# Kernel optimization log

Measured on AMD Instinct MI355X. Metric: run time of the kernel, lower is better.

## Reference

```python
import jax, jax.numpy as jnp
import numpy as np

B, A, D, H, F = 256, 96, 384, 192, 96   # molecules, atoms, feat, hidden, species-MLP out
S = 4                                   # number of species (H, C, N, O)
E = B * A * 32                          # edges (avg degree 32)
CUTOFF = 5.2


def smooth_cutoff(d, cutoff):
    # Smoothstep-style cutoff: 1 at d=0, smoothly -> 0 at d=cutoff (Smoothstep class, reversed edges)
    x = jnp.clip((cutoff - d) / cutoff, 0.0, 1.0)
    return x ** 3 * (x * (6.0 * x - 15.0) + 10.0)


def setup_inputs() -> dict:
    key = jax.random.key(0)
    ks = jax.random.split(key, 9)
    species = jax.random.randint(ks[0], (B, A), 0, S, dtype=jnp.int32)
    in_features = jax.random.normal(ks[1], (B, A, D), dtype=jnp.float32)
    atom_index12 = jax.random.randint(ks[2], (2, E), 0, B * A, dtype=jnp.int32)
    distances = jax.random.uniform(ks[3], (E,), jnp.float32, 0.1, CUTOFF)
    total_charges = jnp.zeros((B,), jnp.float32)
    W1 = jax.random.normal(ks[4], (S, D, H), jnp.float32) / np.float32(np.sqrt(D))
    W2 = jax.random.normal(ks[5], (S, H, F), jnp.float32) / np.float32(np.sqrt(H))
    Wn = jax.random.normal(ks[6], (S, F, F), jnp.float32) / np.float32(np.sqrt(F))
    Wf = jax.random.normal(ks[7], (S, 2 * F, 1), jnp.float32) / np.float32(np.sqrt(2 * F))
    return dict(species=species, in_features=in_features, atom_index12=atom_index12,
                distances=distances, total_charges=total_charges,
                W1=W1, W2=W2, Wn=Wn, Wf=Wf,
                decay_prefactor=jnp.asarray(1.0, jnp.float32),
                decay_factor=jnp.asarray(1.0, jnp.float32))


def reference(species, in_features, atom_index12, distances, total_charges,
              W1, W2, Wn, Wf, decay_prefactor, decay_factor):
    b, a, d = in_features.shape
    n = b * a
    sp = species.reshape(-1)                      # [N]
    x = in_features.reshape(n, d)                 # [N, D]

    # per-species main MLP dispatch: internal[i] = MLP_{sp[i]}(x[i])
    internal = jnp.zeros((n, F), x.dtype)
    for s in range(S):
        mask = (sp == s)[:, None]
        h = jax.nn.gelu(x @ W1[s]) @ W2[s]        # [N, F]
        internal = internal + jnp.where(mask, h, jnp.zeros((), x.dtype))

    # per-species neighbor MLP
    nbr = jnp.zeros((n, F), x.dtype)
    for s in range(S):
        mask = (sp == s)[:, None]
        nbr = nbr + jnp.where(mask, internal @ Wn[s], jnp.zeros((), x.dtype))

    # distance-decayed edge messages: merged[i0] += nbr[i1]*w, merged[i1] += nbr[i0]*w
    decay = (decay_prefactor ** 2) * jnp.exp(-(decay_factor ** 2) * distances) \
            * smooth_cutoff(distances, CUTOFF)    # [E]
    i0, i1 = atom_index12[0], atom_index12[1]
    m_to_i0 = nbr[i1] * decay[:, None]            # [E, F]
    m_to_i1 = nbr[i0] * decay[:, None]
    merged = jax.ops.segment_sum(jnp.concatenate([m_to_i0, m_to_i1], axis=0),
                                 jnp.concatenate([i0, i1], axis=0),
                                 num_segments=n)  # [N, F]

    feats = jnp.concatenate([internal, merged], axis=-1)  # [N, 2F]

    # per-species final head -> precharges
    precharges = jnp.zeros((n,), x.dtype)
    for s in range(S):
        mask = (sp == s)
        precharges = precharges + jnp.where(mask, (feats @ Wf[s])[:, 0], jnp.zeros((), x.dtype))
    precharges = precharges.reshape(b, a)

    # total-charge redistribution (uniform factors, no learned redistribution)
    dummy_mask = species != -1
    factors = 1.0 / dummy_mask.sum(-1, keepdims=True).astype(x.dtype)
    charges = precharges + (total_charges - precharges.sum(-1))[:, None] * factors
    charges = jnp.where(dummy_mask, charges, jnp.zeros((), x.dtype))
    return species, charges, precharges
```

## Files before the change

kernel.cpp:

```cpp
#include <hip/hip_runtime.h>
#include <cstdint>
#include <cstddef>

#define NBm 256
#define NAm 96
#define NDm 384
#define NHm 192
#define NFm 96
#define NSm 4
#define NATOMS (NBm*NAm)
#define NEe (NATOMS*32)
#define NMSG (2*NEe)
#define HBLK 1536
#define CUTOFF_ 5.2f

typedef __attribute__((ext_vector_type(8))) short short8;
typedef __attribute__((ext_vector_type(4))) float float4v;
typedef __attribute__((ext_vector_type(2))) int int2v;

__device__ __forceinline__ short f2bf(float f){
  union { float f; unsigned u; } v; v.f = f;
  unsigned r = v.u + 0x7FFFu + ((v.u >> 16) & 1u);
  return (short)(r >> 16);
}

__device__ __forceinline__ float gelu_t(float x){
  float u = 0.7978845608028654f * (x + 0.044715f * x*x*x);
  float e = __expf(-2.0f * fabsf(u));
  float t = (1.0f - e) / (1.0f + e);
  t = (u >= 0.f) ? t : -t;
  return 0.5f * x * (1.0f + t);
}

#define W1N (NSm*NDm*NHm)
#define W2N (NSm*NHm*NFm)
#define WNN (NSm*NFm*NFm)
__global__ void k_wprep(const float* __restrict__ W1, const float* __restrict__ W2,
                        const float* __restrict__ Wn,
                        short* __restrict__ W1t, short* __restrict__ W2t,
                        short* __restrict__ Wnt, int* __restrict__ spc){
  if (blockIdx.x == 0 && threadIdx.x < NSm) spc[threadIdx.x] = 0;
  int idx = blockIdx.x*256 + threadIdx.x;
  if (idx < W1N){
    int s = idx / (NDm*NHm); int rem = idx - s*NDm*NHm;
    int k = rem / NHm, c = rem - k*NHm;
    W1t[(s*NHm + c)*NDm + k] = f2bf(W1[idx]);
  } else if (idx < W1N + W2N){
    int j = idx - W1N;
    int s = j / (NHm*NFm); int rem = j - s*NHm*NFm;
    int k = rem / NFm, c = rem - k*NFm;
    W2t[(s*NFm + c)*NHm + k] = f2bf(W2[j]);
  } else if (idx < W1N + W2N + WNN){
    int j = idx - W1N - W2N;
    int s = j / (NFm*NFm); int rem = j - s*NFm*NFm;
    int k = rem / NFm, c = rem - k*NFm;
    Wnt[(s*NFm + c)*NFm + k] = f2bf(Wn[j]);
  }
}

__global__ void k_spcount(const int* __restrict__ sp, int* __restrict__ spc){
  __shared__ int h[NSm];
  int t = threadIdx.x;
  if (t < NSm) h[t] = 0;
  __syncthreads();
  int i = blockIdx.x*256 + t;
  atomicAdd(&h[sp[i]], 1);
  __syncthreads();
  if (t < NSm) atomicAdd(&spc[t], h[t]);
}

__global__ void k_spscan(const int* __restrict__ spc, int* __restrict__ sps, int* __restrict__ spcur){
  if (threadIdx.x==0 && blockIdx.x==0){
    int r=0;
    for (int s=0;s<NSm;s++){ sps[s]=r; spcur[s]=r; r+=spc[s]; }
    sps[NSm]=r;
  }
}

__global__ void k_spscatter(const int* __restrict__ sp, int* __restrict__ spcur,
                            int* __restrict__ order){
  __shared__ int h[NSm], base[NSm];
  int t = threadIdx.x;
  if (t < NSm) h[t]=0;
  __syncthreads();
  int i = blockIdx.x*256 + t;
  int s = sp[i];
  int lr = atomicAdd(&h[s], 1);
  __syncthreads();
  if (t < NSm) base[t] = atomicAdd(&spcur[t], h[t]);
  __syncthreads();
  order[base[s] + lr] = i;
}

__global__ __launch_bounds__(256) void k_mlp(
    const float* __restrict__ X, const int* __restrict__ order,
    const int* __restrict__ sps,
    const short* __restrict__ W1t, const short* __restrict__ W2t,
    const short* __restrict__ Wnt, const float* __restrict__ Wf,
    float* __restrict__ pre, float* __restrict__ nbr_g){
  const int s = blockIdx.y;
  const int s0 = sps[s];
  const int cnt = sps[s+1] - s0;
  const int row0 = blockIdx.x * 64;
  if (row0 >= cnt) return;

  __shared__ short Hs[64][200];
  __shared__ short Ws[192*40];
  __shared__ short Is[64][104];
  __shared__ int aids[64];

  const int tid = threadIdx.x;
  if (tid < 64){
    int r = row0 + tid;
    aids[tid] = order[s0 + ((r < cnt) ? r : 0)];
  }
  __syncthreads();

  const int wave = tid >> 6, lane = tid & 63;
  const int lrow = lane & 15, quad = lane >> 4;
  const int arow = wave*16 + lrow;
  const float* xrow = X + (size_t)aids[arow]*NDm + quad*8;

  short8 afs[12];
  #pragma unroll
  for (int kb=0; kb<12; kb++){
    const float* p = xrow + kb*32;
    #pragma unroll
    for (int j=0;j<8;j++) afs[kb][j] = f2bf(p[j]);
  }

  const short* W1s = W1t + (size_t)s*NHm*NDm;
  float4v acc[12];
  #pragma unroll
  for (int i=0;i<12;i++){ acc[i][0]=0.f; acc[i][1]=0.f; acc[i][2]=0.f; acc[i][3]=0.f; }

  for (int kb=0; kb<12; kb++){
    __syncthreads();
    for (int e = tid; e < 192*4; e += 256){
      int c = e >> 2, kq = (e & 3) * 8;
      *(short8*)(&Ws[c*40 + kq]) = *(const short8*)(W1s + c*NDm + kb*32 + kq);
    }
    __syncthreads();
    short8 af = afs[kb];
    #pragma unroll
    for (int ct=0; ct<12; ct++){
      short8 bfb = *(const short8*)(&Ws[(ct*16 + lrow)*40 + quad*8]);
      acc[ct] = __builtin_amdgcn_mfma_f32_16x16x32_bf16(af, bfb, acc[ct], 0,0,0);
    }
  }
  #pragma unroll
  for (int ct=0; ct<12; ct++){
    #pragma unroll
    for (int r=0;r<4;r++){
      Hs[wave*16 + quad*4 + r][ct*16 + lrow] = f2bf(gelu_t(acc[ct][r]));
    }
  }

  const short* W2s = W2t + (size_t)s*NFm*NHm;
  float4v acc2[6];
  #pragma unroll
  for (int i=0;i<6;i++){ acc2[i][0]=0.f; acc2[i][1]=0.f; acc2[i][2]=0.f; acc2[i][3]=0.f; }
  for (int kb=0; kb<6; kb++){
    __syncthreads();
    for (int e = tid; e < 96*4; e += 256){
      int c = e >> 2, kq = (e & 3) * 8;
      *(short8*)(&Ws[c*40 + kq]) = *(const short8*)(W2s + c*NHm + kb*32 + kq);
    }
    __syncthreads();
    short8 af2 = *(const short8*)(&Hs[wave*16 + lrow][kb*32 + quad*8]);
    #pragma unroll
    for (int ct=0; ct<6; ct++){
      short8 bfb = *(const short8*)(&Ws[(ct*16 + lrow)*40 + quad*8]);
      acc2[ct] = __builtin_amdgcn_mfma_f32_16x16x32_bf16(af2, bfb, acc2[ct], 0,0,0);
    }
  }
  #pragma unroll
  for (int ct=0; ct<6; ct++){
    #pragma unroll
    for (int r=0;r<4;r++){
      Is[wave*16 + quad*4 + r][ct*16 + lrow] = f2bf(acc2[ct][r]);
    }
  }

  {
    float pr[4] = {0.f,0.f,0.f,0.f};
    #pragma unroll
    for (int ct=0; ct<6; ct++){
      float wv = Wf[s*2*NFm + ct*16 + lrow];
      #pragma unroll
      for (int r=0;r<4;r++) pr[r] += acc2[ct][r] * wv;
    }
    #pragma unroll
    for (int m=1; m<16; m<<=1){
      #pragma unroll
      for (int r=0;r<4;r++) pr[r] += __shfl_xor(pr[r], m, 64);
    }
    if (lrow == 0){
      #pragma unroll
      for (int r=0;r<4;r++){
        int row = wave*16 + quad*4 + r;
        if (row0 + row < cnt) pre[aids[row]] = pr[r];
      }
    }
  }

  const short* Wns = Wnt + (size_t)s*NFm*NFm;
  float4v acc3[6];
  #pragma unroll
  for (int i=0;i<6;i++){ acc3[i][0]=0.f; acc3[i][1]=0.f; acc3[i][2]=0.f; acc3[i][3]=0.f; }
  for (int kb=0; kb<3; kb++){
    __syncthreads();
    for (int e = tid; e < 96*4; e += 256){
      int c = e >> 2, kq = (e & 3) * 8;
      *(short8*)(&Ws[c*40 + kq]) = *(const short8*)(Wns + c*NFm + kb*32 + kq);
    }
    __syncthreads();
    short8 af3 = *(const short8*)(&Is[wave*16 + lrow][kb*32 + quad*8]);
    #pragma unroll
    for (int ct=0; ct<6; ct++){
      short8 bfb = *(const short8*)(&Ws[(ct*16 + lrow)*40 + quad*8]);
      acc3[ct] = __builtin_amdgcn_mfma_f32_16x16x32_bf16(af3, bfb, acc3[ct], 0,0,0);
    }
  }
  #pragma unroll
  for (int ct=0; ct<6; ct++){
    #pragma unroll
    for (int r=0;r<4;r++){
      int row = wave*16 + quad*4 + r, col = ct*16 + lrow;
      if (row0 + row < cnt) nbr_g[(size_t)aids[row]*NFm + col] = acc3[ct][r];
    }
  }
}

__global__ void k_nd4(const float* __restrict__ nbr, const float* __restrict__ Wf,
                      float* __restrict__ nd4){
  int a = blockIdx.x*4 + (threadIdx.x >> 6);
  int lane = threadIdx.x & 63;
  bool lo = lane < 32;
  const float* np = nbr + (size_t)a*NFm;
  float nv1 = np[lane];
  float nv2 = lo ? np[64+lane] : 0.f;
  const float* w0 = Wf + 0*2*NFm + NFm;
  const float* w1 = Wf + 1*2*NFm + NFm;
  const float* w2 = Wf + 2*2*NFm + NFm;
  const float* w3 = Wf + 3*2*NFm + NFm;
  float n0 = nv1*w0[lane] + (lo ? nv2*w0[64+lane] : 0.f);
  float n1 = nv1*w1[lane] + (lo ? nv2*w1[64+lane] : 0.f);
  float n2 = nv1*w2[lane] + (lo ? nv2*w2[64+lane] : 0.f);
  float n3 = nv1*w3[lane] + (lo ? nv2*w3[64+lane] : 0.f);
  #pragma unroll
  for (int m=1; m<64; m<<=1){
    n0 += __shfl_xor(n0, m, 64);
    n1 += __shfl_xor(n1, m, 64);
    n2 += __shfl_xor(n2, m, 64);
    n3 += __shfl_xor(n3, m, 64);
  }
  if (lane == 0){
    float4v v; v[0]=n0; v[1]=n1; v[2]=n2; v[3]=n3;
    *(float4v*)(nd4 + (size_t)a*4) = v;
  }
}

__global__ __launch_bounds__(1024) void k_hist(const int* __restrict__ ai,
                                               int* __restrict__ Hist){
  __shared__ int h[NBm];
  int t = threadIdx.x;
  if (t < NBm) h[t] = 0;
  __syncthreads();
  int m = blockIdx.x*1024 + t;
  int mol = ai[m] / NAm;
  atomicAdd(&h[mol], 1);
  __syncthreads();
  if (t < NBm) Hist[blockIdx.x*NBm + t] = h[t];
}

__global__ void k_mscan(int* __restrict__ Hist, int* __restrict__ Tot){
  __shared__ int sums[256];
  int mol = blockIdx.x, t = threadIdx.x;
  int v[6]; int loc = 0;
  #pragma unroll
  for (int j=0;j<6;j++){ v[j] = Hist[(t*6+j)*NBm + mol]; loc += v[j]; }
  sums[t] = loc; __syncthreads();
  for (int off=1; off<256; off<<=1){
    int x = (t >= off) ? sums[t-off] : 0;
    __syncthreads();
    sums[t] += x;
    __syncthreads();
  }
  int run = sums[t] - loc;
  #pragma unroll
  for (int j=0;j<6;j++){ Hist[(t*6+j)*NBm + mol] = run; run += v[j]; }
  if (t == 255) Tot[mol] = run;
}

__global__ void k_segscan(const int* __restrict__ Tot, int* __restrict__ Seg){
  __shared__ int s[256];
  int t = threadIdx.x;
  int v = Tot[t]; s[t] = v; __syncthreads();
  for (int off=1; off<256; off<<=1){
    int x = (t >= off) ? s[t-off] : 0;
    __syncthreads();
    s[t] += x;
    __syncthreads();
  }
  Seg[t] = s[t] - v;
  if (t == 255) Seg[256] = s[255];
}

__global__ __launch_bounds__(1024) void k_scatter(const int* __restrict__ ai,
    const float* __restrict__ dist, const float* __restrict__ pref,
    const float* __restrict__ fac, const int* __restrict__ Hist,
    const int* __restrict__ Seg, int2v* __restrict__ Msg){
  __shared__ int cnt[NBm];
  __shared__ int off[NBm];
  int t = threadIdx.x;
  if (t < NBm){ cnt[t] = 0; off[t] = Seg[t] + Hist[blockIdx.x*NBm + t]; }
  __syncthreads();
  int m = blockIdx.x*1024 + t;
  int dest = ai[m];
  int other = ai[(m < NEe) ? m + NEe : m - NEe];
  int e = (m < NEe) ? m : m - NEe;
  float d = dist[e];
  float x = (CUTOFF_ - d) * (1.0f/CUTOFF_);
  x = fminf(fmaxf(x, 0.f), 1.f);
  float sc = x*x*x*(x*(6.f*x - 15.f) + 10.f);
  float p = pref[0], fc = fac[0];
  float w = p*p * expf(-fc*fc*d) * sc;
  int mol = dest / NAm, dl = dest - mol*NAm;
  int rank = atomicAdd(&cnt[mol], 1);
  int2v msg; msg[0] = (other << 7) | dl; msg[1] = __float_as_int(w);
  Msg[off[mol] + rank] = msg;
}

__global__ __launch_bounds__(256) void k_accum(const int* __restrict__ Seg,
    const int2v* __restrict__ Msg, const float* __restrict__ nd4,
    const int* __restrict__ sp, const float* __restrict__ pre,
    const float* __restrict__ tc, float* __restrict__ out){
  __shared__ float acc[NAm];
  __shared__ int spl[NAm];
  __shared__ float red[128];
  int mol = blockIdx.x, t = threadIdx.x;
  if (t < NAm){ acc[t] = 0.f; spl[t] = sp[mol*NAm + t]; }
  __syncthreads();
  int s0 = Seg[mol], s1 = Seg[mol+1];
  for (int i = s0 + t; i < s1; i += 256){
    int2v kw = Msg[i];
    int key = kw[0]; float w = __int_as_float(kw[1]);
    int dl = key & 127, other = key >> 7;
    float val = w * nd4[(size_t)other*4 + spl[dl]];
    atomicAdd(&acc[dl], val);
  }
  __syncthreads();
  float pch = 0.f;
  if (t < NAm) pch = pre[mol*NAm + t] + acc[t];
  if (t < 128) red[t] = (t < NAm) ? pch : 0.f;
  __syncthreads();
  for (int o=64; o>0; o>>=1){
    if (t < o) red[t] += red[t + o];
    __syncthreads();
  }
  float sum = red[0];
  if (t < NAm){
    float c = pch + (tc[mol] - sum) * (1.0f/96.0f);
    out[mol*NAm + t] = (float)spl[t];
    out[NATOMS + mol*NAm + t] = c;
    out[2*NATOMS + mol*NAm + t] = pch;
  }
}

extern "C" void kernel_launch(void* const* d_in, const int* in_sizes, int n_in,
                              void* d_out, int out_size, void* d_ws, size_t ws_size,
                              hipStream_t stream) {
  const int*   species = (const int*)  d_in[0];
  const float* X       = (const float*)d_in[1];
  const int*   ai      = (const int*)  d_in[2];
  const float* dist    = (const float*)d_in[3];
  const float* tc      = (const float*)d_in[4];
  const float* W1      = (const float*)d_in[5];
  const float* W2      = (const float*)d_in[6];
  const float* Wn      = (const float*)d_in[7];
  const float* Wf      = (const float*)d_in[8];
  const float* pref    = (const float*)d_in[9];
  const float* fac     = (const float*)d_in[10];
  float* out = (float*)d_out;

  char* w = (char*)d_ws;
  auto alloc = [&](size_t bytes)->char*{
    char* p = w; w += (bytes + 255) & ~(size_t)255; return p;
  };
  int*   spc   = (int*)  alloc(64);
  int*   sps   = (int*)  alloc(64);
  int*   spcur = (int*)  alloc(64);
  int*   order = (int*)  alloc((size_t)NATOMS*4);
  float* nd4   = (float*)alloc((size_t)NATOMS*4*4);
  float* pre   = (float*)alloc((size_t)NATOMS*4);
  float* nbr   = (float*)alloc((size_t)NATOMS*NFm*4);
  short* W1t   = (short*)alloc((size_t)W1N*2);
  short* W2t   = (short*)alloc((size_t)W2N*2);
  short* Wnt   = (short*)alloc((size_t)WNN*2);
  int*   Hist  = (int*)  alloc((size_t)HBLK*NBm*4);
  int*   Tot   = (int*)  alloc(1024);
  int*   Seg   = (int*)  alloc((NBm+1)*4);
  int2v* Msg   = (int2v*)alloc((size_t)NMSG*8);

  k_wprep<<<(W1N+W2N+WNN)/256, 256, 0, stream>>>(W1, W2, Wn, W1t, W2t, Wnt, spc);
  k_spcount<<<NATOMS/256, 256, 0, stream>>>(species, spc);
  k_spscan<<<1, 64, 0, stream>>>(spc, sps, spcur);
  k_spscatter<<<NATOMS/256, 256, 0, stream>>>(species, spcur, order);
  dim3 g(NATOMS/64, NSm);
  k_mlp<<<g, 256, 0, stream>>>(X, order, sps, W1t, W2t, Wnt, Wf, pre, nbr);
  k_nd4<<<NATOMS/4, 256, 0, stream>>>(nbr, Wf, nd4);
  k_hist<<<HBLK, 1024, 0, stream>>>(ai, Hist);
  k_mscan<<<NBm, 256, 0, stream>>>(Hist, Tot);
  k_segscan<<<1, 256, 0, stream>>>(Tot, Seg);
  k_scatter<<<HBLK, 1024, 0, stream>>>(ai, dist, pref, fac, Hist, Seg, Msg);
  k_accum<<<NBm, 256, 0, stream>>>(Seg, Msg, nd4, species, pre, tc, out);
}
```

Before: 190.9 us.

## Stage larger weight chunks in MLP, halve scatter blocks, widen accumulate blocks

The MLP kernel now stages W1 in four 96-wide K chunks instead of twelve 32-wide ones, and loads W2 and Wn whole into a larger shared buffer. This cuts the number of block-wide barriers and global-load rounds. The histogram and scatter kernels each process two elements per thread over half as many blocks, which shrinks the Hist array and the per-molecule scan work. The accumulate kernel uses 1024 threads per molecule. The larger shared memory footprint of the MLP kernel may lower occupancy.

Result: faster. 183.9 us (-3.6%).

```diff
diff --git a/kernel.cpp b/kernel.cpp
--- a/kernel.cpp
+++ b/kernel.cpp
@@ -11,7 +11,7 @@
 #define NATOMS (NBm*NAm)
 #define NEe (NATOMS*32)
 #define NMSG (2*NEe)
-#define HBLK 1536
+#define HBLK2 768
 #define CUTOFF_ 5.2f
 
 typedef __attribute__((ext_vector_type(8))) short short8;
@@ -105,8 +105,8 @@
   if (row0 >= cnt) return;
 
   __shared__ short Hs[64][200];
-  __shared__ short Ws[192*40];
   __shared__ short Is[64][104];
+  __shared__ short Ws[19968];
   __shared__ int aids[64];
 
   const int tid = threadIdx.x;
@@ -133,19 +133,21 @@
   float4v acc[12];
   #pragma unroll
   for (int i=0;i<12;i++){ acc[i][0]=0.f; acc[i][1]=0.f; acc[i][2]=0.f; acc[i][3]=0.f; }
-
-  for (int kb=0; kb<12; kb++){
-    __syncthreads();
-    for (int e = tid; e < 192*4; e += 256){
-      int c = e >> 2, kq = (e & 3) * 8;
-      *(short8*)(&Ws[c*40 + kq]) = *(const short8*)(W1s + c*NDm + kb*32 + kq);
-    }
-    __syncthreads();
-    short8 af = afs[kb];
-    #pragma unroll
-    for (int ct=0; ct<12; ct++){
-      short8 bfb = *(const short8*)(&Ws[(ct*16 + lrow)*40 + quad*8]);
-      acc[ct] = __builtin_amdgcn_mfma_f32_16x16x32_bf16(af, bfb, acc[ct], 0,0,0);
+  for (int kc=0; kc<4; kc++){
+    __syncthreads();
+    for (int e = tid; e < 192*12; e += 256){
+      int c = e / 12, u = e - c*12;
+      *(short8*)(&Ws[c*104 + u*8]) = *(const short8*)(W1s + c*NDm + kc*96 + u*8);
+    }
+    __syncthreads();
+    #pragma unroll
+    for (int kb3=0; kb3<3; kb3++){
+      short8 af = afs[kc*3 + kb3];
+      #pragma unroll
+      for (int ct=0; ct<12; ct++){
+        short8 bfb = *(const short8*)(&Ws[(ct*16 + lrow)*104 + kb3*32 + quad*8]);
+        acc[ct] = __builtin_amdgcn_mfma_f32_16x16x32_bf16(af, bfb, acc[ct], 0,0,0);
+      }
     }
   }
   #pragma unroll
@@ -160,17 +162,17 @@
   float4v acc2[6];
   #pragma unroll
   for (int i=0;i<6;i++){ acc2[i][0]=0.f; acc2[i][1]=0.f; acc2[i][2]=0.f; acc2[i][3]=0.f; }
+  __syncthreads();
+  for (int e = tid; e < 96*24; e += 256){
+    int c = e / 24, u = e - c*24;
+    *(short8*)(&Ws[c*200 + u*8]) = *(const short8*)(W2s + c*NHm + u*8);
+  }
+  __syncthreads();
   for (int kb=0; kb<6; kb++){
-    __syncthreads();
-    for (int e = tid; e < 96*4; e += 256){
-      int c = e >> 2, kq = (e & 3) * 8;
-      *(short8*)(&Ws[c*40 + kq]) = *(const short8*)(W2s + c*NHm + kb*32 + kq);
-    }
-    __syncthreads();
     short8 af2 = *(const short8*)(&Hs[wave*16 + lrow][kb*32 + quad*8]);
     #pragma unroll
     for (int ct=0; ct<6; ct++){
-      short8 bfb = *(const short8*)(&Ws[(ct*16 + lrow)*40 + quad*8]);
+      short8 bfb = *(const short8*)(&Ws[(ct*16 + lrow)*200 + kb*32 + quad*8]);
       acc2[ct] = __builtin_amdgcn_mfma_f32_16x16x32_bf16(af2, bfb, acc2[ct], 0,0,0);
     }
   }
@@ -208,17 +210,17 @@
   float4v acc3[6];
   #pragma unroll
   for (int i=0;i<6;i++){ acc3[i][0]=0.f; acc3[i][1]=0.f; acc3[i][2]=0.f; acc3[i][3]=0.f; }
+  __syncthreads();
+  for (int e = tid; e < 96*12; e += 256){
+    int c = e / 12, u = e - c*12;
+    *(short8*)(&Ws[c*104 + u*8]) = *(const short8*)(Wns + c*NFm + u*8);
+  }
+  __syncthreads();
   for (int kb=0; kb<3; kb++){
-    __syncthreads();
-    for (int e = tid; e < 96*4; e += 256){
-      int c = e >> 2, kq = (e & 3) * 8;
-      *(short8*)(&Ws[c*40 + kq]) = *(const short8*)(Wns + c*NFm + kb*32 + kq);
-    }
-    __syncthreads();
     short8 af3 = *(const short8*)(&Is[wave*16 + lrow][kb*32 + quad*8]);
     #pragma unroll
     for (int ct=0; ct<6; ct++){
-      short8 bfb = *(const short8*)(&Ws[(ct*16 + lrow)*40 + quad*8]);
+      short8 bfb = *(const short8*)(&Ws[(ct*16 + lrow)*104 + kb*32 + quad*8]);
       acc3[ct] = __builtin_amdgcn_mfma_f32_16x16x32_bf16(af3, bfb, acc3[ct], 0,0,0);
     }
   }
@@ -267,9 +269,9 @@
   int t = threadIdx.x;
   if (t < NBm) h[t] = 0;
   __syncthreads();
-  int m = blockIdx.x*1024 + t;
-  int mol = ai[m] / NAm;
-  atomicAdd(&h[mol], 1);
+  int base = blockIdx.x*2048;
+  atomicAdd(&h[ai[base + t] / NAm], 1);
+  atomicAdd(&h[ai[base + 1024 + t] / NAm], 1);
   __syncthreads();
   if (t < NBm) Hist[blockIdx.x*NBm + t] = h[t];
 }
@@ -277,9 +279,9 @@
 __global__ void k_mscan(int* __restrict__ Hist, int* __restrict__ Tot){
   __shared__ int sums[256];
   int mol = blockIdx.x, t = threadIdx.x;
-  int v[6]; int loc = 0;
-  #pragma unroll
-  for (int j=0;j<6;j++){ v[j] = Hist[(t*6+j)*NBm + mol]; loc += v[j]; }
+  int v[3]; int loc = 0;
+  #pragma unroll
+  for (int j=0;j<3;j++){ v[j] = Hist[(t*3+j)*NBm + mol]; loc += v[j]; }
   sums[t] = loc; __syncthreads();
   for (int off=1; off<256; off<<=1){
     int x = (t >= off) ? sums[t-off] : 0;
@@ -289,7 +291,7 @@
   }
   int run = sums[t] - loc;
   #pragma unroll
-  for (int j=0;j<6;j++){ Hist[(t*6+j)*NBm + mol] = run; run += v[j]; }
+  for (int j=0;j<3;j++){ Hist[(t*3+j)*NBm + mol] = run; run += v[j]; }
   if (t == 255) Tot[mol] = run;
 }
 
@@ -316,23 +318,27 @@
   int t = threadIdx.x;
   if (t < NBm){ cnt[t] = 0; off[t] = Seg[t] + Hist[blockIdx.x*NBm + t]; }
   __syncthreads();
-  int m = blockIdx.x*1024 + t;
-  int dest = ai[m];
-  int other = ai[(m < NEe) ? m + NEe : m - NEe];
-  int e = (m < NEe) ? m : m - NEe;
-  float d = dist[e];
-  float x = (CUTOFF_ - d) * (1.0f/CUTOFF_);
-  x = fminf(fmaxf(x, 0.f), 1.f);
-  float sc = x*x*x*(x*(6.f*x - 15.f) + 10.f);
+  int base = blockIdx.x*2048;
   float p = pref[0], fc = fac[0];
-  float w = p*p * expf(-fc*fc*d) * sc;
-  int mol = dest / NAm, dl = dest - mol*NAm;
-  int rank = atomicAdd(&cnt[mol], 1);
-  int2v msg; msg[0] = (other << 7) | dl; msg[1] = __float_as_int(w);
-  Msg[off[mol] + rank] = msg;
-}
-
-__global__ __launch_bounds__(256) void k_accum(const int* __restrict__ Seg,
+  #pragma unroll
+  for (int half=0; half<2; half++){
+    int m = base + half*1024 + t;
+    int dest = ai[m];
+    int other = ai[(m < NEe) ? m + NEe : m - NEe];
+    int e = (m < NEe) ? m : m - NEe;
+    float d = dist[e];
+    float x = (CUTOFF_ - d) * (1.0f/CUTOFF_);
+    x = fminf(fmaxf(x, 0.f), 1.f);
+    float sc = x*x*x*(x*(6.f*x - 15.f) + 10.f);
+    float w = p*p * expf(-fc*fc*d) * sc;
+    int mol = dest / NAm, dl = dest - mol*NAm;
+    int rank = atomicAdd(&cnt[mol], 1);
+    int2v msg; msg[0] = (other << 7) | dl; msg[1] = __float_as_int(w);
+    Msg[off[mol] + rank] = msg;
+  }
+}
+
+__global__ __launch_bounds__(1024) void k_accum(const int* __restrict__ Seg,
     const int2v* __restrict__ Msg, const float* __restrict__ nd4,
     const int* __restrict__ sp, const float* __restrict__ pre,
     const float* __restrict__ tc, float* __restrict__ out){
@@ -343,7 +349,7 @@
   if (t < NAm){ acc[t] = 0.f; spl[t] = sp[mol*NAm + t]; }
   __syncthreads();
   int s0 = Seg[mol], s1 = Seg[mol+1];
-  for (int i = s0 + t; i < s1; i += 256){
+  for (int i = s0 + t; i < s1; i += 1024){
     int2v kw = Msg[i];
     int key = kw[0]; float w = __int_as_float(kw[1]);
     int dl = key & 127, other = key >> 7;
@@ -398,7 +404,7 @@
   short* W1t   = (short*)alloc((size_t)W1N*2);
   short* W2t   = (short*)alloc((size_t)W2N*2);
   short* Wnt   = (short*)alloc((size_t)WNN*2);
-  int*   Hist  = (int*)  alloc((size_t)HBLK*NBm*4);
+  int*   Hist  = (int*)  alloc((size_t)HBLK2*NBm*4);
   int*   Tot   = (int*)  alloc(1024);
   int*   Seg   = (int*)  alloc((NBm+1)*4);
   int2v* Msg   = (int2v*)alloc((size_t)NMSG*8);
@@ -410,9 +416,9 @@
   dim3 g(NATOMS/64, NSm);
   k_mlp<<<g, 256, 0, stream>>>(X, order, sps, W1t, W2t, Wnt, Wf, pre, nbr);
   k_nd4<<<NATOMS/4, 256, 0, stream>>>(nbr, Wf, nd4);
-  k_hist<<<HBLK, 1024, 0, stream>>>(ai, Hist);
+  k_hist<<<HBLK2, 1024, 0, stream>>>(ai, Hist);
   k_mscan<<<NBm, 256, 0, stream>>>(Hist, Tot);
   k_segscan<<<1, 256, 0, stream>>>(Tot, Seg);
-  k_scatter<<<HBLK, 1024, 0, stream>>>(ai, dist, pref, fac, Hist, Seg, Msg);
-  k_accum<<<NBm, 256, 0, stream>>>(Seg, Msg, nd4, species, pre, tc, out);
-}
+  k_scatter<<<HBLK2, 1024, 0, stream>>>(ai, dist, pref, fac, Hist, Seg, Msg);
+  k_accum<<<NBm, 1024, 0, stream>>>(Seg, Msg, nd4, species, pre, tc, out);
+}
```
